# Kernel optimization log

Hardware: AMD Instinct MI355X
Metric: run time of the kernel (lower is better)

Reference implementation:

```python
import jax, jax.numpy as jnp
import numpy as np
from jax import lax

VOCAB = 32000
EMB = 512
HID = 1024
BATCH = 64
MAX_LEN = 30
STEPS = MAX_LEN + 2
SOS = 1
PAD = 0


def setup_inputs() -> dict:
    key = jax.random.key(0)
    ks = jax.random.split(key, 9)
    s = 0.05
    target = jax.random.randint(ks[0], (BATCH, 1), 0, VOCAB)
    encoder_hidden = jax.random.normal(ks[1], (1, BATCH, HID), dtype=jnp.float32)
    emb = jax.random.normal(ks[2], (VOCAB, EMB), dtype=jnp.float32) * s
    emb = emb.at[PAD].set(0.0)  # padding_idx row zeroed like torch
    W_ih = jax.random.normal(ks[3], (3 * HID, EMB), dtype=jnp.float32) * s
    W_hh = jax.random.normal(ks[4], (3 * HID, HID), dtype=jnp.float32) * s
    b_ih = jax.random.normal(ks[5], (3 * HID,), dtype=jnp.float32) * s
    b_hh = jax.random.normal(ks[6], (3 * HID,), dtype=jnp.float32) * s
    fc_W = jax.random.normal(ks[7], (VOCAB, HID), dtype=jnp.float32) * s
    fc_b = jax.random.normal(ks[8], (VOCAB,), dtype=jnp.float32) * s
    return {"target": target, "encoder_hidden": encoder_hidden, "emb": emb,
            "W_ih": W_ih, "W_hh": W_hh, "b_ih": b_ih, "b_hh": b_hh,
            "fc_W": fc_W, "fc_b": fc_b}


def reference(target, encoder_hidden, emb, W_ih, W_hh, b_ih, b_hh, fc_W, fc_b):
    B = target.shape[0]

    def step(carry, _):
        tok, h = carry                      # tok [B] int, h [B,H]
        x = emb[tok]                        # [B,E] embedding lookup
        gi = x @ W_ih.T + b_ih              # [B,3H]
        gh = h @ W_hh.T + b_hh              # [B,3H]
        i_r, i_z, i_n = jnp.split(gi, 3, axis=-1)
        h_r, h_z, h_n = jnp.split(gh, 3, axis=-1)
        r = jax.nn.sigmoid(i_r + h_r)
        z = jax.nn.sigmoid(i_z + h_z)
        n = jnp.tanh(i_n + r * h_n)
        h_new = (1.0 - z) * n + z * h       # torch GRU update
        logits = h_new @ fc_W.T + fc_b      # [B,V]
        logp = jax.nn.log_softmax(logits, axis=-1)
        tok_new = jnp.argmax(logp, axis=-1)  # greedy feedback (topk, k=1)
        return (tok_new, h_new), logp

    h0 = encoder_hidden[0]                  # num_layers == 1
    tok0 = jnp.full((B,), SOS, dtype=jnp.int32)
    (_, hT), outs = lax.scan(step, (tok0, h0), None, length=STEPS)
    decoder_outputs = jnp.transpose(outs, (1, 0, 2))  # [B, STEPS, V]
    return decoder_outputs, hT[None]
```

## Files before the change

kernel.cpp:

```cpp
#include <hip/hip_runtime.h>

#define VV 32000
#define EE 512
#define HH 1024
#define NB 64
#define NSTEP 32

typedef __attribute__((ext_vector_type(8))) short short8;
typedef __attribute__((ext_vector_type(4))) float f32x4;
typedef unsigned long long u64;

#define MFMA16(a, b, c) __builtin_amdgcn_mfma_f32_16x16x32_bf16((a), (b), (c), 0, 0, 0)

__device__ __forceinline__ unsigned short f2bf(float f) {
  unsigned int u = __float_as_uint(f);
  u += 0x7fffu + ((u >> 16) & 1u);
  return (unsigned short)(u >> 16);
}
__device__ __forceinline__ float bf2f(unsigned short b) {
  return __uint_as_float(((unsigned int)b) << 16);
}
__device__ __forceinline__ float sigmoidf_(float x) { return 1.0f / (1.0f + expf(-x)); }
__device__ __forceinline__ unsigned int ordkey(float f) {
  unsigned int u = __float_as_uint(f);
  return u ^ ((u >> 31) ? 0xFFFFFFFFu : 0x80000000u);
}
__device__ __forceinline__ float ordkey_inv(unsigned int u) {
  return __uint_as_float((u & 0x80000000u) ? (u ^ 0x80000000u) : ~u);
}

__global__ __launch_bounds__(256) void prep_wcat(const float* __restrict__ Wih,
                                                 const float* __restrict__ Whh,
                                                 unsigned short* __restrict__ wm,
                                                 unsigned short* __restrict__ wr) {
  int ub = blockIdx.x / 3, g = blockIdx.x % 3;
  for (int e = threadIdx.x; e < 48 * 512; e += 256) {
    int ks = e >> 9, lane = (e >> 3) & 63, j = e & 7;
    int row = g * HH + ub * 16 + (lane & 15);
    int k = ks * 32 + ((lane >> 4) << 3) + j;
    float f = (k < EE) ? Wih[(size_t)row * EE + k] : Whh[(size_t)row * HH + (k - EE)];
    unsigned short m_ = f2bf(f);
    size_t idx = (((size_t)(ub * 3 + g) * 48 + ks) * 64 + lane) * 8 + j;
    wm[idx] = m_;
    wr[idx] = f2bf(f - bf2f(m_));
  }
}

__global__ __launch_bounds__(256) void prep_wfc(const float* __restrict__ fcW,
                                                unsigned short* __restrict__ wfc) {
  int vg = blockIdx.x;
  for (int e = threadIdx.x; e < 32768; e += 256) {
    int ks = e >> 10, n = (e >> 9) & 1, lane = (e >> 3) & 63, j = e & 7;
    int v = vg * 32 + n * 16 + (lane & 15);
    int k = ks * 32 + ((lane >> 4) << 3) + j;
    wfc[(((size_t)vg * 32 + ks) * 2 + n) * 512 + lane * 8 + j] = f2bf(fcW[(size_t)v * HH + k]);
  }
}

__global__ __launch_bounds__(256) void init_kernel(
    const float* __restrict__ enc, const float* __restrict__ emb, float* __restrict__ h4a,
    unsigned short* __restrict__ ham, unsigned short* __restrict__ har,
    unsigned short* __restrict__ xam, unsigned short* __restrict__ xar,
    int* __restrict__ cnt) {
  int i = blockIdx.x * 256 + threadIdx.x;
  int b = i >> 10, u = i & 1023;
  float hv = enc[i];
  h4a[i] = hv;
  unsigned short m_ = f2bf(hv);
  size_t idx = (((size_t)(b >> 4) * 32 + (u >> 5)) * 64 + ((b & 15) + (((u >> 3) & 3) << 4))) * 8 + (u & 7);
  ham[idx] = m_;
  har[idx] = f2bf(hv - bf2f(m_));
  if (i < NB * EE) {
    int b2 = i >> 9, k = i & 511;
    float xv = emb[EE + k];
    unsigned short xm = f2bf(xv);
    size_t xi = (((size_t)(b2 >> 4) * 16 + (k >> 5)) * 64 + ((b2 & 15) + (((k >> 3) & 3) << 4))) * 8 + (k & 7);
    xam[xi] = xm;
    xar[xi] = f2bf(xv - bf2f(xm));
  }
  if (i < NB) cnt[i] = 0;
}

__device__ __forceinline__ void gru_body(
    int bid, int tid, float (*red)[16][65],
    const unsigned short* xam, const unsigned short* xar,
    const unsigned short* him, const unsigned short* hir,
    const float* h4in, float* h4out,
    const unsigned short* wm, const unsigned short* wrs,
    const float* bih, const float* bhh,
    unsigned short* hom, unsigned short* hor) {
  const int lane = tid & 63, w = tid >> 6;
  const int ub = bid >> 2, mg = bid & 3;
  f32x4 aR{}, aZ{}, aNX{}, aNH{};
  const short8* XM = (const short8*)xam;
  const short8* XR = (const short8*)xar;
  const short8* HM = (const short8*)him;
  const short8* HR = (const short8*)hir;
  const short8* WM = (const short8*)wm;
  const short8* WR = (const short8*)wrs;
#pragma unroll
  for (int s = 0; s < 12; ++s) {
    int ks = w * 12 + s;
    short8 am, ar;
    if (ks < 16) {
      int o = (mg * 16 + ks) * 64 + lane;
      am = XM[o]; ar = XR[o];
    } else {
      int o = (mg * 32 + (ks - 16)) * 64 + lane;
      am = HM[o]; ar = HR[o];
    }
    {
      int o = ((ub * 3 + 0) * 48 + ks) * 64 + lane;
      short8 wmv = WM[o], wrv = WR[o];
      aR = MFMA16(am, wmv, aR); aR = MFMA16(ar, wmv, aR); aR = MFMA16(am, wrv, aR);
    }
    {
      int o = ((ub * 3 + 1) * 48 + ks) * 64 + lane;
      short8 wmv = WM[o], wrv = WR[o];
      aZ = MFMA16(am, wmv, aZ); aZ = MFMA16(ar, wmv, aZ); aZ = MFMA16(am, wrv, aZ);
    }
    {
      int o = ((ub * 3 + 2) * 48 + ks) * 64 + lane;
      short8 wmv = WM[o], wrv = WR[o];
      if (ks < 16) {
        aNX = MFMA16(am, wmv, aNX); aNX = MFMA16(ar, wmv, aNX); aNX = MFMA16(am, wrv, aNX);
      } else {
        aNH = MFMA16(am, wmv, aNH); aNH = MFMA16(ar, wmv, aNH); aNH = MFMA16(am, wrv, aNH);
      }
    }
  }
#pragma unroll
  for (int reg = 0; reg < 4; ++reg) {
    int rr = ((lane >> 4) << 2) + reg, c = lane & 15;
    red[w][rr][c] = aR[reg];
    red[w][rr][16 + c] = aZ[reg];
    red[w][rr][32 + c] = aNX[reg];
    red[w][rr][48 + c] = aNH[reg];
  }
  __syncthreads();
  const int mrow = tid >> 4, uu = tid & 15;
  float R = 0.f, Z = 0.f, NX = 0.f, NH = 0.f;
#pragma unroll
  for (int q = 0; q < 4; ++q) {
    R += red[q][mrow][uu];
    Z += red[q][mrow][16 + uu];
    NX += red[q][mrow][32 + uu];
    NH += red[q][mrow][48 + uu];
  }
  const int b = mg * 16 + mrow, u = ub * 16 + uu;
  float r = sigmoidf_(R + bih[u] + bhh[u]);
  float z = sigmoidf_(Z + bih[HH + u] + bhh[HH + u]);
  float n = tanhf(NX + bih[2 * HH + u] + r * (NH + bhh[2 * HH + u]));
  float hold = h4in[b * HH + u];
  float hn = (1.0f - z) * n + z * hold;
  h4out[b * HH + u] = hn;
  unsigned short m_ = f2bf(hn);
  size_t idx = (((size_t)(b >> 4) * 32 + (u >> 5)) * 64 + ((b & 15) + (((u >> 3) & 3) << 4))) * 8 + (u & 7);
  hom[idx] = m_;
  hor[idx] = f2bf(hn - bf2f(m_));
}

__global__ __launch_bounds__(256, 4) void gru_kernel(
    const unsigned short* xam, const unsigned short* xar,
    const unsigned short* him, const unsigned short* hir,
    const float* h4in, float* h4out,
    const unsigned short* wm, const unsigned short* wrs,
    const float* bih, const float* bhh,
    unsigned short* hom, unsigned short* hor) {
  __shared__ float red[4][16][65];
  gru_body(blockIdx.x, threadIdx.x, red, xam, xar, him, hir, h4in, h4out, wm, wrs, bih, bhh, hom, hor);
}

__global__ __launch_bounds__(256, 8) void fc_kernel(
    const unsigned short* __restrict__ ham,
    const unsigned short* __restrict__ wfc, const float* __restrict__ fcb,
    float* __restrict__ out, u64* __restrict__ blkkeys, int t) {
  const int tid = threadIdx.x;
  const int lane = tid & 63, w = tid >> 6;
  const int vg = blockIdx.x;
  f32x4 acc0{}, acc1{};
  const short8* HM = (const short8*)ham + (size_t)w * 2048;
  const short8* W = (const short8*)wfc + (size_t)vg * 4096;
#pragma unroll 8
  for (int ks = 0; ks < 32; ++ks) {
    short8 am = HM[ks * 64 + lane];
    short8 w0 = W[(ks * 2 + 0) * 64 + lane];
    short8 w1 = W[(ks * 2 + 1) * 64 + lane];
    acc0 = MFMA16(am, w0, acc0);
    acc1 = MFMA16(am, w1, acc1);
  }
  const int r0 = lane >> 4, c0 = lane & 15;
  const float b0 = fcb[vg * 32 + c0];
  const float b1 = fcb[vg * 32 + 16 + c0];
  u64 kk[4];
#pragma unroll
  for (int reg = 0; reg < 4; ++reg) {
    const int b = w * 16 + r0 * 4 + reg;
    float v0 = acc0[reg] + b0;
    float v1 = acc1[reg] + b1;
    size_t ro = ((size_t)b * NSTEP + t) * VV + (size_t)vg * 32 + c0;
    out[ro] = v0;
    out[ro + 16] = v1;
    u64 k0 = ((u64)ordkey(v0) << 32) | (u64)(0xFFFFFFFFu - (unsigned)(vg * 32 + c0));
    u64 k1 = ((u64)ordkey(v1) << 32) | (u64)(0xFFFFFFFFu - (unsigned)(vg * 32 + 16 + c0));
    kk[reg] = k0 > k1 ? k0 : k1;
  }
#pragma unroll
  for (int d = 1; d < 16; d <<= 1)
#pragma unroll
    for (int reg = 0; reg < 4; ++reg) {
      u64 o = __shfl_xor(kk[reg], d, 64);
      if (o > kk[reg]) kk[reg] = o;
    }
  if (c0 == 0) {
#pragma unroll
    for (int reg = 0; reg < 4; ++reg)
      blkkeys[(size_t)(w * 16 + r0 * 4 + reg) * 1000 + vg] = kk[reg];
  }
}

__global__ __launch_bounds__(256) void sel1_kernel(
    const float* __restrict__ out, const u64* __restrict__ blkkeys,
    int* __restrict__ cnt, int* __restrict__ cand, int t) {
  const int b = blockIdx.x >> 3, q = blockIdx.x & 7;
  const int tid = threadIdx.x;
  __shared__ u64 skey[256];
  const u64* kb = blkkeys + (size_t)b * 1000;
  u64 mk = 0;
  for (int i = tid; i < 1000; i += 256) {
    u64 k = kb[i];
    if (k > mk) mk = k;
  }
  skey[tid] = mk;
  __syncthreads();
  for (int off = 128; off > 0; off >>= 1) {
    if (tid < off && skey[tid + off] > skey[tid]) skey[tid] = skey[tid + off];
    __syncthreads();
  }
  const float Mf = ordkey_inv((unsigned)(skey[0] >> 32));
  const float thr = Mf - 0.10f;
  const float* rowp = out + ((size_t)b * NSTEP + t) * VV;
  for (int v = q * (VV / 8) + tid; v < (q + 1) * (VV / 8); v += 256) {
    if (rowp[v] >= thr) {
      int p = atomicAdd(&cnt[b], 1);
      if (p < 256) cand[b * 256 + p] = v;
    }
  }
}

__global__ __launch_bounds__(256) void sel2_kernel(
    int* __restrict__ cnt, const int* __restrict__ cand,
    const float* __restrict__ fcW, const float* __restrict__ fcb,
    const float* __restrict__ emb, const float* __restrict__ h4,
    unsigned short* __restrict__ xam, unsigned short* __restrict__ xar) {
  const int b = blockIdx.x, tid = threadIdx.x;
  __shared__ int scand[256];
  __shared__ u64 rkey[256];
  __shared__ int stok;
  int n = cnt[b];
  if (n > 256) n = 256;
  for (int i = tid; i < n; i += 256) scand[i] = cand[b * 256 + i];
  __syncthreads();
  const int w = tid >> 6, ln = tid & 63;
  for (int ci = w; ci < n; ci += 4) {
    int v = scand[ci];
    float p = 0.f;
#pragma unroll
    for (int q = 0; q < 16; ++q)
      p += h4[b * HH + ln + (q << 6)] * fcW[(size_t)v * HH + ln + (q << 6)];
#pragma unroll
    for (int d = 1; d < 64; d <<= 1) p += __shfl_xor(p, d);
    if (ln == 0)
      rkey[ci] = ((u64)ordkey(p + fcb[v]) << 32) | (u64)(0xFFFFFFFFu - (unsigned)v);
  }
  __syncthreads();
  if (tid == 0) {
    u64 bk = 0;
    for (int ci = 0; ci < n; ++ci)
      if (rkey[ci] > bk) bk = rkey[ci];
    stok = (int)(0xFFFFFFFFu - (unsigned)(bk & 0xFFFFFFFFu));
    cnt[b] = 0;
  }
  __syncthreads();
  const int tok = stok;
  for (int k = tid; k < EE; k += 256) {
    float xv = emb[(size_t)tok * EE + k];
    unsigned short xm = f2bf(xv);
    size_t xi = (((size_t)(b >> 4) * 16 + (k >> 5)) * 64 + ((b & 15) + (((k >> 3) & 3) << 4))) * 8 + (k & 7);
    xam[xi] = xm;
    xar[xi] = f2bf(xv - bf2f(xm));
  }
}

__global__ __launch_bounds__(256) void lsm_kernel(float* __restrict__ out) {
  const int bt = blockIdx.x;
  const int tid = threadIdx.x;
  float* row = out + (size_t)bt * VV;
  float4* r4 = (float4*)row;
  __shared__ float mred[256], sred[256];
  float m = -INFINITY, s = 0.f;
  for (int i = tid; i < VV / 4; i += 256) {
    float4 v = r4[i];
#pragma unroll
    for (int c = 0; c < 4; ++c) {
      float x = (&v.x)[c];
      if (x > m) { s = s * expf(m - x) + 1.0f; m = x; }
      else s += expf(x - m);
    }
  }
  mred[tid] = m; sred[tid] = s;
  __syncthreads();
  for (int off = 128; off > 0; off >>= 1) {
    if (tid < off) {
      float m1 = mred[tid], s1 = sred[tid];
      float m2 = mred[tid + off], s2 = sred[tid + off];
      float M = fmaxf(m1, m2);
      mred[tid] = M;
      sred[tid] = s1 * expf(m1 - M) + s2 * expf(m2 - M);
    }
    __syncthreads();
  }
  const float lse = mred[0] + logf(sred[0]);
  for (int i = tid; i < VV / 4; i += 256) {
    float4 v = r4[i];
    v.x -= lse; v.y -= lse; v.z -= lse; v.w -= lse;
    r4[i] = v;
  }
}

__global__ __launch_bounds__(256) void final_kernel(const float* __restrict__ h4,
                                                    float* __restrict__ out) {
  int i = blockIdx.x * 256 + threadIdx.x;
  out[(size_t)NB * NSTEP * VV + i] = h4[i];
}

extern "C" void kernel_launch(void* const* d_in, const int* in_sizes, int n_in,
                              void* d_out, int out_size, void* d_ws, size_t ws_size,
                              hipStream_t stream) {
  const float* enc = (const float*)d_in[1];
  const float* emb = (const float*)d_in[2];
  const float* Wih = (const float*)d_in[3];
  const float* Whh = (const float*)d_in[4];
  const float* bih = (const float*)d_in[5];
  const float* bhh = (const float*)d_in[6];
  const float* fcW = (const float*)d_in[7];
  const float* fcb = (const float*)d_in[8];
  float* out = (float*)d_out;

  char* ws = (char*)d_ws;
  unsigned short* wfc = (unsigned short*)ws; ws += (size_t)32768000 * 2;
  unsigned short* wcm = (unsigned short*)ws; ws += (size_t)4718592 * 2;
  unsigned short* wcr = (unsigned short*)ws; ws += (size_t)4718592 * 2;
  unsigned short* hAm = (unsigned short*)ws; ws += (size_t)65536 * 2;
  unsigned short* hAr = (unsigned short*)ws; ws += (size_t)65536 * 2;
  unsigned short* hBm = (unsigned short*)ws; ws += (size_t)65536 * 2;
  unsigned short* hBr = (unsigned short*)ws; ws += (size_t)65536 * 2;
  unsigned short* xam = (unsigned short*)ws; ws += (size_t)32768 * 2;
  unsigned short* xar = (unsigned short*)ws; ws += (size_t)32768 * 2;
  float* h4a = (float*)ws; ws += (size_t)NB * HH * 4;
  float* h4b = (float*)ws; ws += (size_t)NB * HH * 4;
  u64* blkkeys = (u64*)ws; ws += (size_t)NB * 1000 * 8;
  int* cnt = (int*)ws; ws += (size_t)NB * 4;
  int* cand = (int*)ws; ws += (size_t)NB * 256 * 4;

  prep_wfc<<<1000, 256, 0, stream>>>(fcW, wfc);
  prep_wcat<<<192, 256, 0, stream>>>(Wih, Whh, wcm, wcr);
  init_kernel<<<256, 256, 0, stream>>>(enc, emb, h4a, hAm, hAr, xam, xar, cnt);

  for (int t = 0; t < NSTEP; ++t) {
    const float* hin = (t & 1) ? h4b : h4a;
    float* hout = (t & 1) ? h4a : h4b;
    const unsigned short* him = (t & 1) ? hBm : hAm;
    const unsigned short* hir = (t & 1) ? hBr : hAr;
    unsigned short* hom = (t & 1) ? hAm : hBm;
    unsigned short* hor = (t & 1) ? hAr : hBr;
    gru_kernel<<<256, 256, 0, stream>>>(xam, xar, him, hir, hin, hout, wcm, wcr, bih, bhh, hom, hor);
    fc_kernel<<<1000, 256, 0, stream>>>(hom, wfc, fcb, out, blkkeys, t);
    sel1_kernel<<<512, 256, 0, stream>>>(out, blkkeys, cnt, cand, t);
    sel2_kernel<<<64, 256, 0, stream>>>(cnt, cand, fcW, fcb, emb, hout, xam, xar);
  }
  lsm_kernel<<<2048, 256, 0, stream>>>(out);
  final_kernel<<<256, 256, 0, stream>>>(h4a, out);
}
```

Measured before the change: 1.829 ms.

## Store logits as bf16 and fuse candidate selection kernels via arrival counter

The fc kernel now writes logits to a bf16 scratch buffer instead of fp32 output, which halves write traffic and the reads in the threshold scan and the final log-softmax. The two selection kernels are merged into one: the last block to arrive per batch row does the exact fp32 rescoring and embedding update, and the counters are reset with atomics. The final hidden-state copy is folded into the log-softmax launch. As a trade-off, the emitted log-probabilities inherit bf16 rounding error, which may exceed the output tolerance.

New measurement: 1.709 ms. -6.6%, faster.

```diff
diff --git a/kernel.cpp b/kernel.cpp
--- a/kernel.cpp
+++ b/kernel.cpp
@@ -61,7 +61,7 @@
     const float* __restrict__ enc, const float* __restrict__ emb, float* __restrict__ h4a,
     unsigned short* __restrict__ ham, unsigned short* __restrict__ har,
     unsigned short* __restrict__ xam, unsigned short* __restrict__ xar,
-    int* __restrict__ cnt) {
+    int* __restrict__ cnt, int* __restrict__ arrive) {
   int i = blockIdx.x * 256 + threadIdx.x;
   int b = i >> 10, u = i & 1023;
   float hv = enc[i];
@@ -78,7 +78,7 @@
     xam[xi] = xm;
     xar[xi] = f2bf(xv - bf2f(xm));
   }
-  if (i < NB) cnt[i] = 0;
+  if (i < NB) { cnt[i] = 0; arrive[i] = 0; }
 }
 
 __device__ __forceinline__ void gru_body(
@@ -174,7 +174,7 @@
 __global__ __launch_bounds__(256, 8) void fc_kernel(
     const unsigned short* __restrict__ ham,
     const unsigned short* __restrict__ wfc, const float* __restrict__ fcb,
-    float* __restrict__ out, u64* __restrict__ blkkeys, int t) {
+    unsigned short* __restrict__ lgb, u64* __restrict__ blkkeys, int t) {
   const int tid = threadIdx.x;
   const int lane = tid & 63, w = tid >> 6;
   const int vg = blockIdx.x;
@@ -199,8 +199,8 @@
     float v0 = acc0[reg] + b0;
     float v1 = acc1[reg] + b1;
     size_t ro = ((size_t)b * NSTEP + t) * VV + (size_t)vg * 32 + c0;
-    out[ro] = v0;
-    out[ro + 16] = v1;
+    lgb[ro] = f2bf(v0);
+    lgb[ro + 16] = f2bf(v1);
     u64 k0 = ((u64)ordkey(v0) << 32) | (u64)(0xFFFFFFFFu - (unsigned)(vg * 32 + c0));
     u64 k1 = ((u64)ordkey(v1) << 32) | (u64)(0xFFFFFFFFu - (unsigned)(vg * 32 + 16 + c0));
     kk[reg] = k0 > k1 ? k0 : k1;
@@ -219,12 +219,18 @@
   }
 }
 
-__global__ __launch_bounds__(256) void sel1_kernel(
-    const float* __restrict__ out, const u64* __restrict__ blkkeys,
-    int* __restrict__ cnt, int* __restrict__ cand, int t) {
+__global__ __launch_bounds__(256) void sel_kernel(
+    const unsigned short* __restrict__ lgb, const u64* __restrict__ blkkeys,
+    int* __restrict__ cnt, int* __restrict__ cand, int* __restrict__ arrive,
+    const float* __restrict__ fcW, const float* __restrict__ fcb,
+    const float* __restrict__ emb, const float* __restrict__ h4,
+    unsigned short* __restrict__ xam, unsigned short* __restrict__ xar, int t) {
   const int b = blockIdx.x >> 3, q = blockIdx.x & 7;
   const int tid = threadIdx.x;
   __shared__ u64 skey[256];
+  __shared__ int slast, stok;
+  __shared__ u64 rkey[256];
+
   const u64* kb = blkkeys + (size_t)b * 1000;
   u64 mk = 0;
   for (int i = tid; i < 1000; i += 256) {
@@ -239,35 +245,33 @@
   }
   const float Mf = ordkey_inv((unsigned)(skey[0] >> 32));
   const float thr = Mf - 0.10f;
-  const float* rowp = out + ((size_t)b * NSTEP + t) * VV;
-  for (int v = q * (VV / 8) + tid; v < (q + 1) * (VV / 8); v += 256) {
-    if (rowp[v] >= thr) {
-      int p = atomicAdd(&cnt[b], 1);
-      if (p < 256) cand[b * 256 + p] = v;
-    }
-  }
-}
-
-__global__ __launch_bounds__(256) void sel2_kernel(
-    int* __restrict__ cnt, const int* __restrict__ cand,
-    const float* __restrict__ fcW, const float* __restrict__ fcb,
-    const float* __restrict__ emb, const float* __restrict__ h4,
-    unsigned short* __restrict__ xam, unsigned short* __restrict__ xar) {
-  const int b = blockIdx.x, tid = threadIdx.x;
-  __shared__ int scand[256];
-  __shared__ u64 rkey[256];
-  __shared__ int stok;
-  int n = cnt[b];
+
+  const short8* r8v = (const short8*)(lgb + ((size_t)b * NSTEP + t) * VV);
+  for (int i = q * 500 + tid; i < (q + 1) * 500; i += 256) {
+    short8 v8 = r8v[i];
+#pragma unroll
+    for (int e = 0; e < 8; ++e) {
+      float x = bf2f((unsigned short)v8[e]);
+      if (x >= thr) {
+        int p = atomicAdd(&cnt[b], 1);
+        if (p < 256) atomicExch(&cand[b * 256 + p], i * 8 + e);
+      }
+    }
+  }
+  __syncthreads();
+  if (tid == 0) slast = (atomicAdd(&arrive[b], 1) == 7) ? 1 : 0;
+  __syncthreads();
+  if (!slast) return;
+
+  int n = atomicAdd(&cnt[b], 0);
   if (n > 256) n = 256;
-  for (int i = tid; i < n; i += 256) scand[i] = cand[b * 256 + i];
-  __syncthreads();
   const int w = tid >> 6, ln = tid & 63;
   for (int ci = w; ci < n; ci += 4) {
-    int v = scand[ci];
+    int v = atomicAdd(&cand[b * 256 + ci], 0);
     float p = 0.f;
 #pragma unroll
-    for (int q = 0; q < 16; ++q)
-      p += h4[b * HH + ln + (q << 6)] * fcW[(size_t)v * HH + ln + (q << 6)];
+    for (int qq = 0; qq < 16; ++qq)
+      p += h4[b * HH + ln + (qq << 6)] * fcW[(size_t)v * HH + ln + (qq << 6)];
 #pragma unroll
     for (int d = 1; d < 64; d <<= 1) p += __shfl_xor(p, d);
     if (ln == 0)
@@ -279,9 +283,11 @@
     for (int ci = 0; ci < n; ++ci)
       if (rkey[ci] > bk) bk = rkey[ci];
     stok = (int)(0xFFFFFFFFu - (unsigned)(bk & 0xFFFFFFFFu));
-    cnt[b] = 0;
-  }
-  __syncthreads();
+    atomicExch(&cnt[b], 0);
+    atomicExch(&arrive[b], 0);
+  }
+  __syncthreads();
+
   const int tok = stok;
   for (int k = tid; k < EE; k += 256) {
     float xv = emb[(size_t)tok * EE + k];
@@ -292,18 +298,25 @@
   }
 }
 
-__global__ __launch_bounds__(256) void lsm_kernel(float* __restrict__ out) {
-  const int bt = blockIdx.x;
+__global__ __launch_bounds__(256) void lsm_kernel(const unsigned short* __restrict__ lgb,
+                                                  const float* __restrict__ h4,
+                                                  float* __restrict__ out) {
+  const int bid = blockIdx.x;
   const int tid = threadIdx.x;
-  float* row = out + (size_t)bt * VV;
-  float4* r4 = (float4*)row;
+  if (bid >= 2048) {
+    int i = (bid - 2048) * 256 + tid;
+    out[(size_t)NB * NSTEP * VV + i] = h4[i];
+    return;
+  }
+  const short8* r8v = (const short8*)(lgb + (size_t)bid * VV);
+  float* orow = out + (size_t)bid * VV;
   __shared__ float mred[256], sred[256];
   float m = -INFINITY, s = 0.f;
-  for (int i = tid; i < VV / 4; i += 256) {
-    float4 v = r4[i];
-#pragma unroll
-    for (int c = 0; c < 4; ++c) {
-      float x = (&v.x)[c];
+  for (int i = tid; i < VV / 8; i += 256) {
+    short8 v8 = r8v[i];
+#pragma unroll
+    for (int c = 0; c < 8; ++c) {
+      float x = bf2f((unsigned short)v8[c]);
       if (x > m) { s = s * expf(m - x) + 1.0f; m = x; }
       else s += expf(x - m);
     }
@@ -321,17 +334,20 @@
     __syncthreads();
   }
   const float lse = mred[0] + logf(sred[0]);
-  for (int i = tid; i < VV / 4; i += 256) {
-    float4 v = r4[i];
-    v.x -= lse; v.y -= lse; v.z -= lse; v.w -= lse;
-    r4[i] = v;
-  }
-}
-
-__global__ __launch_bounds__(256) void final_kernel(const float* __restrict__ h4,
-                                                    float* __restrict__ out) {
-  int i = blockIdx.x * 256 + threadIdx.x;
-  out[(size_t)NB * NSTEP * VV + i] = h4[i];
+  for (int i = tid; i < VV / 8; i += 256) {
+    short8 v8 = r8v[i];
+    float4 o0, o1;
+    o0.x = bf2f((unsigned short)v8[0]) - lse;
+    o0.y = bf2f((unsigned short)v8[1]) - lse;
+    o0.z = bf2f((unsigned short)v8[2]) - lse;
+    o0.w = bf2f((unsigned short)v8[3]) - lse;
+    o1.x = bf2f((unsigned short)v8[4]) - lse;
+    o1.y = bf2f((unsigned short)v8[5]) - lse;
+    o1.z = bf2f((unsigned short)v8[6]) - lse;
+    o1.w = bf2f((unsigned short)v8[7]) - lse;
+    ((float4*)orow)[i * 2] = o0;
+    ((float4*)orow)[i * 2 + 1] = o1;
+  }
 }
 
 extern "C" void kernel_launch(void* const* d_in, const int* in_sizes, int n_in,
@@ -361,11 +377,13 @@
   float* h4b = (float*)ws; ws += (size_t)NB * HH * 4;
   u64* blkkeys = (u64*)ws; ws += (size_t)NB * 1000 * 8;
   int* cnt = (int*)ws; ws += (size_t)NB * 4;
+  int* arrive = (int*)ws; ws += (size_t)NB * 4;
   int* cand = (int*)ws; ws += (size_t)NB * 256 * 4;
+  unsigned short* lgb = (unsigned short*)ws; ws += (size_t)NB * NSTEP * VV * 2;
 
   prep_wfc<<<1000, 256, 0, stream>>>(fcW, wfc);
   prep_wcat<<<192, 256, 0, stream>>>(Wih, Whh, wcm, wcr);
-  init_kernel<<<256, 256, 0, stream>>>(enc, emb, h4a, hAm, hAr, xam, xar, cnt);
+  init_kernel<<<256, 256, 0, stream>>>(enc, emb, h4a, hAm, hAr, xam, xar, cnt, arrive);
 
   for (int t = 0; t < NSTEP; ++t) {
     const float* hin = (t & 1) ? h4b : h4a;
@@ -375,10 +393,8 @@
     unsigned short* hom = (t & 1) ? hAm : hBm;
     unsigned short* hor = (t & 1) ? hAr : hBr;
     gru_kernel<<<256, 256, 0, stream>>>(xam, xar, him, hir, hin, hout, wcm, wcr, bih, bhh, hom, hor);
-    fc_kernel<<<1000, 256, 0, stream>>>(hom, wfc, fcb, out, blkkeys, t);
-    sel1_kernel<<<512, 256, 0, stream>>>(out, blkkeys, cnt, cand, t);
-    sel2_kernel<<<64, 256, 0, stream>>>(cnt, cand, fcW, fcb, emb, hout, xam, xar);
-  }
-  lsm_kernel<<<2048, 256, 0, stream>>>(out);
-  final_kernel<<<256, 256, 0, stream>>>(h4a, out);
-}
+    fc_kernel<<<1000, 256, 0, stream>>>(hom, wfc, fcb, lgb, blkkeys, t);
+    sel_kernel<<<512, 256, 0, stream>>>(lgb, blkkeys, cnt, cand, arrive, fcW, fcb, emb, hout, xam, xar, t);
+  }
+  lsm_kernel<<<2304, 256, 0, stream>>>(lgb, h4a, out);
+}
```
